# Performance work log

Measured on AMD Instinct MI355X. Metric: run time of the kernel, lower is better.

Reference implementation:

```python
import jax, jax.numpy as jnp
import numpy as np

DIM = 256
NUM_HEADS = 8
HEAD_DIM = DIM // NUM_HEADS
NUM_MAIN = 2
NUM_MOD = 4
SEQ_MAIN = 1536
SEQ_AUX = 768
BS = 2


def setup_inputs() -> dict:
    key = jax.random.key(0)
    ks = jax.random.split(key, 6)
    x0 = jax.random.normal(ks[0], (BS, SEQ_MAIN, DIM), jnp.float32)
    x1 = jax.random.normal(ks[1], (BS, SEQ_MAIN, DIM), jnp.float32)
    x2 = jax.random.normal(ks[2], (BS, SEQ_AUX, DIM), jnp.float32)
    x3 = jax.random.normal(ks[3], (BS, SEQ_AUX, DIM), jnp.float32)
    Wqkv = jax.random.normal(ks[4], (NUM_MOD, DIM, 3 * DIM), jnp.float32) * 0.02
    bqkv = jnp.zeros((NUM_MOD, 3 * DIM), jnp.float32)
    Wproj = jax.random.normal(ks[5], (NUM_MOD, DIM, DIM), jnp.float32) * 0.02
    bproj = jnp.zeros((NUM_MOD, DIM), jnp.float32)
    return {"x0": x0, "x1": x1, "x2": x2, "x3": x3,
            "Wqkv": Wqkv, "bqkv": bqkv, "Wproj": Wproj, "bproj": bproj}


def _split_qkv(qkv):
    bs, s, _ = qkv.shape
    qkv = qkv.reshape(bs, s, 3, NUM_HEADS, HEAD_DIM).transpose(2, 0, 3, 1, 4)
    return qkv[0], qkv[1], qkv[2]


def _sdpa(q, k, v):
    scale = 1.0 / jnp.sqrt(jnp.asarray(HEAD_DIM, q.dtype))
    scores = jnp.einsum('bhqd,bhkd->bhqk', q, k) * scale
    probs = jax.nn.softmax(scores, axis=-1)
    return jnp.einsum('bhqk,bhkd->bhqd', probs, v)


def _merge_heads(t):
    # [bs, heads, s, head_dim] -> [bs, s, dim]
    bs, h, s, d = t.shape
    return t.transpose(0, 2, 1, 3).reshape(bs, s, h * d)


def reference(x0, x1, x2, x3, Wqkv, bqkv, Wproj, bproj):
    xs = [x0, x1, x2, x3]
    seqlens = [x.shape[1] for x in xs]
    qs, ks, vs = [], [], []
    for i in range(NUM_MOD):
        q, k, v = _split_qkv(xs[i] @ Wqkv[i] + bqkv[i])
        qs.append(q); ks.append(k); vs.append(v)

    main_q = jnp.concatenate(qs[:NUM_MAIN], axis=2)
    main_k = jnp.concatenate(ks[:NUM_MAIN], axis=2)
    main_v = jnp.concatenate(vs[:NUM_MAIN], axis=2)
    main_x = _merge_heads(_sdpa(main_q, main_k, main_v))  # [bs, sum(main seqlens), dim]
    splits = np.cumsum(seqlens[:NUM_MAIN])[:-1]
    outs = list(jnp.split(main_x, splits, axis=1))

    # aux modalities attend over detached main KV + own KV
    mk = jax.lax.stop_gradient(main_k)
    mv = jax.lax.stop_gradient(main_v)
    for i in range(NUM_MAIN, NUM_MOD):
        k = jnp.concatenate([mk, ks[i]], axis=2)
        v = jnp.concatenate([mv, vs[i]], axis=2)
        outs.append(_merge_heads(_sdpa(qs[i], k, v)))

    outs = [outs[i] @ Wproj[i] + bproj[i] for i in range(NUM_MOD)]
    # concatenate per-modality outputs along the sequence dim for a single output
    return jnp.concatenate(outs, axis=1)
```

## Files before the change

### kernel.cpp

```cpp
#include <hip/hip_runtime.h>
#include <hip/hip_bf16.h>
#include <math.h>

#define BS 2
#define NHEADS 8
#define HD 32
#define DIM 256
#define W3 768
#define S_MAIN 1536
#define S_AUX 768
#define SM_TOT 3072
#define S_TOT 4608

typedef _Float16 f16x8 __attribute__((ext_vector_type(8)));
typedef _Float16 f16x4 __attribute__((ext_vector_type(4)));
typedef float    f32x4 __attribute__((ext_vector_type(4)));

#define QK_SCALE 0.25503491f

#define QM_H  0
#define KM_H  1572864
#define VMT_H 3145728
#define QA_H  4718592
#define KA_H  5505024
#define VAT_H 6291456
#define XH_H  7077888
#define AO0_F 3538944
#define AO1_F 5898240
#define L0_F  8257536
#define L1_F  8266752
#define WT1_H 16551936
#define WT2_H 17338368

#define GLOAD_LDS(SRC, DST)                                                    \
    __builtin_amdgcn_global_load_lds(                                          \
        (const __attribute__((address_space(1))) void*)(SRC),                  \
        (__attribute__((address_space(3))) void*)(DST), 16, 0, 0)

__global__ __launch_bounds__(256) void convert_kernel(
    const float* __restrict__ x0, const float* __restrict__ x1,
    const float* __restrict__ x2, const float* __restrict__ x3,
    const float* __restrict__ Wqkv, const float* __restrict__ Wproj,
    _Float16* __restrict__ wsh)
{
    const int bid = blockIdx.x;
    const int t   = threadIdx.x;

    if (bid < 1152) {
        const float* src;
        int off;
        if (bid < 384)      { src = x0; off = (bid      ) * 2048; }
        else if (bid < 768) { src = x1 - 786432 + 0;  off = bid * 2048; }
        else if (bid < 960) { src = x2; off = 1572864 + (bid - 768) * 2048; }
        else                { src = x3; off = 1966080 + (bid - 960) * 2048; }
        const int base = (bid < 384) ? bid * 2048
                       : (bid < 768) ? (bid - 384) * 2048
                       : (bid < 960) ? (bid - 768) * 2048
                       : (bid - 960) * 2048;
        const float* p = ((bid < 384) ? x0 : (bid < 768) ? x1
                         : (bid < 960) ? x2 : x3) + base + t * 8;
        _Float16* dst = wsh + XH_H + off + t * 8;
        const float4 u0 = *(const float4*)(p + 0);
        const float4 u1 = *(const float4*)(p + 4);
        f16x8 h;
        h[0] = (_Float16)u0.x; h[1] = (_Float16)u0.y;
        h[2] = (_Float16)u0.z; h[3] = (_Float16)u0.w;
        h[4] = (_Float16)u1.x; h[5] = (_Float16)u1.y;
        h[6] = (_Float16)u1.z; h[7] = (_Float16)u1.w;
        *(f16x8*)dst = h;
    } else if (bid < 1200) {
        const int i  = bid - 1152;
        const int m  = i / 12;
        const int cc = i % 12;
        const int col = cc * 64 + (t & 63);
        const int kq  = t >> 6;
        const float* Wm = Wqkv + m * (DIM * W3);
        _Float16*   Wt  = wsh + WT1_H + m * (W3 * DIM) + col * DIM;
        #pragma unroll 4
        for (int k = kq * 64; k < kq * 64 + 64; ++k)
            Wt[k] = (_Float16)Wm[k * W3 + col];
    } else {
        const int i  = bid - 1200;
        const int m  = i / 4;
        const int cc = i % 4;
        const int col = cc * 64 + (t & 63);
        const int kq  = t >> 6;
        const float* Wm = Wproj + m * (DIM * DIM);
        _Float16*   Wt  = wsh + WT2_H + m * (DIM * DIM) + col * DIM;
        #pragma unroll 4
        for (int k = kq * 64; k < kq * 64 + 64; ++k)
            Wt[k] = (_Float16)Wm[k * DIM + col];
    }
}

__global__ __launch_bounds__(256) void qkv_mfma_kernel(
    const _Float16* __restrict__ wsh_ro, const float* __restrict__ bqkv,
    _Float16* __restrict__ wsh)
{
    const int m  = blockIdx.z;
    const int rt = blockIdx.y;
    const int ct = blockIdx.x;
    const int s_m   = (m < 2) ? S_MAIN : S_AUX;
    const int nrows = BS * s_m;
    const int r0 = rt * 128;
    if (r0 >= nrows) return;

    const int xoff = (m == 0) ? 0 : (m == 1) ? 786432
                   : (m == 2) ? 1572864 : 1966080;
    const _Float16* xh = wsh_ro + XH_H + xoff;
    const _Float16* Wt = wsh_ro + WT1_H + m * (W3 * DIM);
    const float* bias  = bqkv + m * W3;

    __shared__ _Float16 As[128][40];
    __shared__ _Float16 Bs[64][40];

    const int t    = threadIdx.x;
    const int wid  = t >> 6;
    const int lane = t & 63;
    const int g    = lane >> 4;
    const int c    = lane & 15;
    const int c0   = ct * 64;

    const int arow = t >> 1;
    const int ak   = (t & 1) << 4;
    const int bcol = t & 63;
    const int bkg  = t >> 6;
    const int bsg  = bkg ^ ((bcol >> 3) & 3);

    f32x4 acc[2][4];
    #pragma unroll
    for (int i = 0; i < 2; ++i)
        #pragma unroll
        for (int j = 0; j < 4; ++j)
            acc[i][j] = (f32x4){0.f, 0.f, 0.f, 0.f};

    const _Float16* xp = xh + (r0 + arow) * DIM + ak;
    const _Float16* wp = Wt + (c0 + bcol) * DIM;

    for (int kk = 0; kk < DIM; kk += 32) {
        {
            const f16x8 h0 = *(const f16x8*)(xp + kk);
            const f16x8 h1 = *(const f16x8*)(xp + kk + 8);
            *(f16x8*)&As[arow][ak]     = h0;
            *(f16x8*)&As[arow][ak + 8] = h1;
        }
        {
            const f16x8 hb = *(const f16x8*)(wp + kk + bkg * 8);
            *(f16x8*)&Bs[bcol][bsg << 3] = hb;
        }
        __syncthreads();
        const f16x8 af0 = *(const f16x8*)&As[wid * 32 + c][g * 8];
        const f16x8 af1 = *(const f16x8*)&As[wid * 32 + 16 + c][g * 8];
        #pragma unroll
        for (int j = 0; j < 4; ++j) {
            const int bc = j * 16 + c;
            const int gg = g ^ ((bc >> 3) & 3);
            const f16x8 bf = *(const f16x8*)&Bs[bc][gg * 8];
            acc[0][j] = __builtin_amdgcn_mfma_f32_16x16x32_f16(af0, bf, acc[0][j], 0, 0, 0);
            acc[1][j] = __builtin_amdgcn_mfma_f32_16x16x32_f16(af1, bf, acc[1][j], 0, 0, 0);
        }
        __syncthreads();
    }

    #pragma unroll
    for (int i = 0; i < 2; ++i) {
        const int gr = r0 + wid * 32 + i * 16 + 4 * g;
        const int b  = (gr >= s_m) ? 1 : 0;
        const int s  = gr - (b ? s_m : 0);
        #pragma unroll
        for (int j = 0; j < 4; ++j) {
            const int col   = c0 + j * 16 + c;
            const int which = col >> 8;
            const int head  = (col >> 5) & 7;
            const int dd    = col & 31;
            const float bv  = bias[col];
            const f32x4 a   = acc[i][j];
            if (which < 2) {
                const float qs = (which == 0) ? QK_SCALE : 1.0f;
                _Float16* dst;
                int base;
                if (m < 2) {
                    dst  = wsh + (which == 0 ? QM_H : KM_H);
                    base = ((b * NHEADS + head) * SM_TOT + (s + m * S_MAIN)) * HD + dd;
                } else {
                    dst  = wsh + (which == 0 ? QA_H : KA_H);
                    base = ((((m - 2) * BS + b) * NHEADS + head) * S_AUX + s) * HD + dd;
                }
                dst[base + 0 * HD] = (_Float16)((a[0] + bv) * qs);
                dst[base + 1 * HD] = (_Float16)((a[1] + bv) * qs);
                dst[base + 2 * HD] = (_Float16)((a[2] + bv) * qs);
                dst[base + 3 * HD] = (_Float16)((a[3] + bv) * qs);
            } else {
                _Float16* dst;
                int base;
                if (m < 2) {
                    dst  = wsh + VMT_H;
                    base = ((b * NHEADS + head) * HD + dd) * SM_TOT + (s + m * S_MAIN);
                } else {
                    dst  = wsh + VAT_H;
                    base = ((((m - 2) * BS + b) * NHEADS + head) * HD + dd) * S_AUX + s;
                }
                f16x4 hv;
                hv[0] = (_Float16)(a[0] + bv);
                hv[1] = (_Float16)(a[1] + bv);
                hv[2] = (_Float16)(a[2] + bv);
                hv[3] = (_Float16)(a[3] + bv);
                *(f16x4*)(dst + base) = hv;
            }
        }
    }
}

__global__ __launch_bounds__(256) void attn_mfma_kernel(
    const _Float16* __restrict__ wsh, float* __restrict__ wsf)
{
    __shared__ _Float16 kbuf[2][64 * 32];
    __shared__ _Float16 vbuf[2][32 * 64];

    const int wid  = threadIdx.x >> 6;
    const int lane = threadIdx.x & 63;
    const int g    = lane >> 4;
    const int c    = lane & 15;

    const int bid = blockIdx.x;

    const _Float16 *qp, *kp0, *vt0, *kp1, *vt1;
    int n0, n1, vs1, orow0, ocol, half;

    if (bid < 384) {
        const int mbhg = bid / 12;
        const int mod  = mbhg >> 4;
        const int b    = (mbhg >> 3) & 1;
        const int h    = mbhg & 7;
        const int t    = bid % 12;
        const int qt   = t >> 1;
        half = t & 1;
        const int q0   = qt * 128 + wid * 32;
        const int mbh  = (mod * BS + b) * NHEADS + h;
        const int bh   = b * NHEADS + h;
        qp = wsh + QA_H + (mbh * S_AUX + q0) * HD;
        if (half == 0) {
            kp0 = wsh + KM_H  + bh * SM_TOT * HD;
            vt0 = wsh + VMT_H + bh * HD * SM_TOT;
            n0  = 1920;
            kp1 = nullptr; vt1 = nullptr; n1 = 0; vs1 = 0;
        } else {
            kp0 = wsh + KM_H  + (bh * SM_TOT + 1920) * HD;
            vt0 = wsh + VMT_H + bh * HD * SM_TOT + 1920;
            n0  = 1152;
            kp1 = wsh + KA_H  + mbh * S_AUX * HD;
            vt1 = wsh + VAT_H + mbh * HD * S_AUX;
            n1  = S_AUX; vs1 = S_AUX;
        }
        orow0 = b * S_TOT + SM_TOT + mod * S_AUX + q0;
        ocol  = h * HD;
    } else {
        const int idx = bid - 384;
        const int bh  = idx / 48;
        const int t   = idx % 48;
        const int qt  = t >> 1;
        half = t & 1;
        const int q0  = qt * 128 + wid * 32;
        const int b = bh >> 3, h = bh & 7;
        const int ks = half * 1536;
        qp  = wsh + QM_H  + (bh * SM_TOT + q0) * HD;
        kp0 = wsh + KM_H  + (bh * SM_TOT + ks) * HD;
        vt0 = wsh + VMT_H + bh * HD * SM_TOT + ks;
        n0  = 1536;
        kp1 = nullptr; vt1 = nullptr; n1 = 0; vs1 = 0;
        orow0 = b * S_TOT + q0;
        ocol  = h * HD;
    }

    const f16x8 qfA = *(const f16x8*)(qp + c * HD + g * 8);
    const f16x8 qfB = *(const f16x8*)(qp + (16 + c) * HD + g * 8);

    const int pc    = ((c >> 2) << 3) + (c & 3);
    const int kchr  = (g ^ (c >> 2)) << 3;
    const int koff0 = pc * HD + kchr;
    const int koff1 = (pc + 4) * HD + kchr;

    const int krow  = wid * 16 + (lane >> 2);
    const int kchg  = ((lane & 3) ^ ((krow >> 3) & 3)) << 3;

    const int srow = wid * 8 + (lane >> 3);
    const int jl   = lane & 7;
    const int vswz = (jl ^ (srow & 7)) << 3;
    const int vr0 = ((g     ^ (c & 7)) << 3);
    const int vr1 = (((g+4) ^ (c & 7)) << 3);

    f16x8 ones;
    #pragma unroll
    for (int i = 0; i < 8; ++i) ones[i] = (_Float16)1.0f;

    f32x4 otA0 = {0.f, 0.f, 0.f, 0.f}, otA1 = {0.f, 0.f, 0.f, 0.f};
    f32x4 otB0 = {0.f, 0.f, 0.f, 0.f}, otB1 = {0.f, 0.f, 0.f, 0.f};
    f32x4 ltA  = {0.f, 0.f, 0.f, 0.f}, ltB  = {0.f, 0.f, 0.f, 0.f};

    int cur = 0;

    #pragma unroll 1
    for (int seg = 0; seg < 2; ++seg) {
        const _Float16* kp_ = seg ? kp1 : kp0;
        const _Float16* vt_ = seg ? vt1 : vt0;
        const int n  = seg ? n1  : n0;
        const int vs = seg ? vs1 : SM_TOT;
        if (n == 0) break;

        #define STAGE(BI, K0)                                                  \
            {                                                                  \
                const _Float16* ks_ = kp_ + (K0 + krow) * HD + kchg;           \
                GLOAD_LDS(ks_, &kbuf[BI][wid * 512]);                          \
                const _Float16* vs_ = vt_ + (K0) + srow * vs + vswz;           \
                GLOAD_LDS(vs_, &vbuf[BI][wid * 512]);                          \
            }

        #define COMPUTE_TILE(BI)                                               \
            {                                                                  \
                const _Float16* kb_ = &kbuf[BI][0];                            \
                const _Float16* vb_ = &vbuf[BI][0];                            \
                const f16x8 kf0 = *(const f16x8*)(kb_ + koff0);                \
                const f16x8 kf1 = *(const f16x8*)(kb_ + koff1);                \
                const f16x8 kf2 = *(const f16x8*)(kb_ + 32 * HD + koff0);      \
                const f16x8 kf3 = *(const f16x8*)(kb_ + 32 * HD + koff1);      \
                const f16x8 va0 = *(const f16x8*)(vb_ + c * 64 + vr0);         \
                const f16x8 va1 = *(const f16x8*)(vb_ + (16 + c) * 64 + vr0);  \
                const f16x8 vb0 = *(const f16x8*)(vb_ + c * 64 + vr1);         \
                const f16x8 vb1 = *(const f16x8*)(vb_ + (16 + c) * 64 + vr1);  \
                f32x4 sA0 = __builtin_amdgcn_mfma_f32_16x16x32_f16(            \
                    kf0, qfA, (f32x4){0.f, 0.f, 0.f, 0.f}, 0, 0, 0);           \
                f32x4 sA1 = __builtin_amdgcn_mfma_f32_16x16x32_f16(            \
                    kf1, qfA, (f32x4){0.f, 0.f, 0.f, 0.f}, 0, 0, 0);           \
                f32x4 sA2 = __builtin_amdgcn_mfma_f32_16x16x32_f16(            \
                    kf2, qfA, (f32x4){0.f, 0.f, 0.f, 0.f}, 0, 0, 0);           \
                f32x4 sA3 = __builtin_amdgcn_mfma_f32_16x16x32_f16(            \
                    kf3, qfA, (f32x4){0.f, 0.f, 0.f, 0.f}, 0, 0, 0);           \
                f32x4 sB0 = __builtin_amdgcn_mfma_f32_16x16x32_f16(            \
                    kf0, qfB, (f32x4){0.f, 0.f, 0.f, 0.f}, 0, 0, 0);           \
                f32x4 sB1 = __builtin_amdgcn_mfma_f32_16x16x32_f16(            \
                    kf1, qfB, (f32x4){0.f, 0.f, 0.f, 0.f}, 0, 0, 0);           \
                f32x4 sB2 = __builtin_amdgcn_mfma_f32_16x16x32_f16(            \
                    kf2, qfB, (f32x4){0.f, 0.f, 0.f, 0.f}, 0, 0, 0);           \
                f32x4 sB3 = __builtin_amdgcn_mfma_f32_16x16x32_f16(            \
                    kf3, qfB, (f32x4){0.f, 0.f, 0.f, 0.f}, 0, 0, 0);           \
                float pA0[4], pA1[4], pA2[4], pA3[4];                          \
                float pB0[4], pB1[4], pB2[4], pB3[4];                          \
                _Pragma("unroll")                                              \
                for (int r = 0; r < 4; ++r) {                                  \
                    pA0[r] = __builtin_amdgcn_exp2f(sA0[r]);                   \
                    pA1[r] = __builtin_amdgcn_exp2f(sA1[r]);                   \
                    pA2[r] = __builtin_amdgcn_exp2f(sA2[r]);                   \
                    pA3[r] = __builtin_amdgcn_exp2f(sA3[r]);                   \
                    pB0[r] = __builtin_amdgcn_exp2f(sB0[r]);                   \
                    pB1[r] = __builtin_amdgcn_exp2f(sB1[r]);                   \
                    pB2[r] = __builtin_amdgcn_exp2f(sB2[r]);                   \
                    pB3[r] = __builtin_amdgcn_exp2f(sB3[r]);                   \
                }                                                              \
                f16x8 pbA0, pbA1, pbB0, pbB1;                                  \
                _Pragma("unroll")                                              \
                for (int r = 0; r < 4; ++r) {                                  \
                    pbA0[r]     = (_Float16)pA0[r];                            \
                    pbA0[r + 4] = (_Float16)pA1[r];                            \
                    pbA1[r]     = (_Float16)pA2[r];                            \
                    pbA1[r + 4] = (_Float16)pA3[r];                            \
                    pbB0[r]     = (_Float16)pB0[r];                            \
                    pbB0[r + 4] = (_Float16)pB1[r];                            \
                    pbB1[r]     = (_Float16)pB2[r];                            \
                    pbB1[r + 4] = (_Float16)pB3[r];                            \
                }                                                              \
                ltA = __builtin_amdgcn_mfma_f32_16x16x32_f16(ones, pbA0, ltA, 0, 0, 0); \
                ltA = __builtin_amdgcn_mfma_f32_16x16x32_f16(ones, pbA1, ltA, 0, 0, 0); \
                ltB = __builtin_amdgcn_mfma_f32_16x16x32_f16(ones, pbB0, ltB, 0, 0, 0); \
                ltB = __builtin_amdgcn_mfma_f32_16x16x32_f16(ones, pbB1, ltB, 0, 0, 0); \
                otA0 = __builtin_amdgcn_mfma_f32_16x16x32_f16(va0, pbA0, otA0, 0, 0, 0); \
                otA1 = __builtin_amdgcn_mfma_f32_16x16x32_f16(va1, pbA0, otA1, 0, 0, 0); \
                otB0 = __builtin_amdgcn_mfma_f32_16x16x32_f16(va0, pbB0, otB0, 0, 0, 0); \
                otB1 = __builtin_amdgcn_mfma_f32_16x16x32_f16(va1, pbB0, otB1, 0, 0, 0); \
                otA0 = __builtin_amdgcn_mfma_f32_16x16x32_f16(vb0, pbA1, otA0, 0, 0, 0); \
                otA1 = __builtin_amdgcn_mfma_f32_16x16x32_f16(vb1, pbA1, otA1, 0, 0, 0); \
                otB0 = __builtin_amdgcn_mfma_f32_16x16x32_f16(vb0, pbB1, otB0, 0, 0, 0); \
                otB1 = __builtin_amdgcn_mfma_f32_16x16x32_f16(vb1, pbB1, otB1, 0, 0, 0); \
            }

        STAGE(cur, 0);
        __syncthreads();

        #pragma unroll 1
        for (int k0 = 0; k0 < n; k0 += 64) {
            if (k0 + 64 < n)
                STAGE(cur ^ 1, k0 + 64);
            COMPUTE_TILE(cur);
            __syncthreads();
            cur ^= 1;
        }

        #undef STAGE
        #undef COMPUTE_TILE
    }

    float* aoBase = wsf + (half ? AO1_F : AO0_F);
    float* lBase  = wsf + (half ? L1_F  : L0_F);

    float* aoA = aoBase + (orow0 + c) * DIM + ocol;
    float* aoB = aoBase + (orow0 + 16 + c) * DIM + ocol;
    float4 w0, w1, w2, w3;
    w0.x = otA0[0]; w0.y = otA0[1]; w0.z = otA0[2]; w0.w = otA0[3];
    w1.x = otA1[0]; w1.y = otA1[1]; w1.z = otA1[2]; w1.w = otA1[3];
    w2.x = otB0[0]; w2.y = otB0[1]; w2.z = otB0[2]; w2.w = otB0[3];
    w3.x = otB1[0]; w3.y = otB1[1]; w3.z = otB1[2]; w3.w = otB1[3];
    *(float4*)(aoA + 4 * g)      = w0;
    *(float4*)(aoA + 16 + 4 * g) = w1;
    *(float4*)(aoB + 4 * g)      = w2;
    *(float4*)(aoB + 16 + 4 * g) = w3;

    if (g == 0) {
        lBase[orow0 + c]      = ltA[0];
        lBase[orow0 + 16 + c] = ltB[0];
    }
}

__global__ __launch_bounds__(256) void proj_mfma_kernel(
    const float* __restrict__ wsf, const _Float16* __restrict__ wsh_ro,
    const float* __restrict__ bproj, float* __restrict__ out)
{
    const int ct = blockIdx.x;
    const int rt = blockIdx.y;
    const int r0 = rt * 128, c0 = ct * 64;
    const int seq = r0 % S_TOT;
    const int mod = (seq < S_MAIN) ? 0 : (seq < SM_TOT) ? 1
                  : (seq < SM_TOT + S_AUX) ? 2 : 3;
    const _Float16* Wt = wsh_ro + WT2_H + mod * (DIM * DIM);
    const float* bias  = bproj + mod * DIM;
    const float* A0    = wsf + AO0_F;
    const float* A1    = wsf + AO1_F;
    const float* L0p   = wsf + L0_F;
    const float* L1p   = wsf + L1_F;

    __shared__ _Float16 As[128][40];
    __shared__ _Float16 Bs[64][40];
    __shared__ float Linv[128];

    const int t    = threadIdx.x;
    const int wid  = t >> 6;
    const int lane = t & 63;
    const int g    = lane >> 4;
    const int c    = lane & 15;

    if (t < 128) Linv[t] = 1.0f / (L0p[r0 + t] + L1p[r0 + t]);
    __syncthreads();

    const int arow = t >> 1;
    const int ak   = (t & 1) << 4;
    const int bcol = t & 63;
    const int bkg  = t >> 6;
    const int bsg  = bkg ^ ((bcol >> 3) & 3);
    const float linv_r = Linv[arow];

    f32x4 acc[2][4];
    #pragma unroll
    for (int i = 0; i < 2; ++i)
        #pragma unroll
        for (int j = 0; j < 4; ++j)
            acc[i][j] = (f32x4){0.f, 0.f, 0.f, 0.f};

    const float* pa0 = A0 + (r0 + arow) * DIM + ak;
    const float* pa1 = A1 + (r0 + arow) * DIM + ak;
    const _Float16* wp = Wt + (c0 + bcol) * DIM;

    for (int kk = 0; kk < DIM; kk += 32) {
        {
            const float4 u0 = *(const float4*)(pa0 + kk + 0);
            const float4 u1 = *(const float4*)(pa0 + kk + 4);
            const float4 u2 = *(const float4*)(pa0 + kk + 8);
            const float4 u3 = *(const float4*)(pa0 + kk + 12);
            const float4 v0 = *(const float4*)(pa1 + kk + 0);
            const float4 v1 = *(const float4*)(pa1 + kk + 4);
            const float4 v2 = *(const float4*)(pa1 + kk + 8);
            const float4 v3 = *(const float4*)(pa1 + kk + 12);
            f16x8 h0, h1;
            h0[0] = (_Float16)((u0.x + v0.x) * linv_r);
            h0[1] = (_Float16)((u0.y + v0.y) * linv_r);
            h0[2] = (_Float16)((u0.z + v0.z) * linv_r);
            h0[3] = (_Float16)((u0.w + v0.w) * linv_r);
            h0[4] = (_Float16)((u1.x + v1.x) * linv_r);
            h0[5] = (_Float16)((u1.y + v1.y) * linv_r);
            h0[6] = (_Float16)((u1.z + v1.z) * linv_r);
            h0[7] = (_Float16)((u1.w + v1.w) * linv_r);
            h1[0] = (_Float16)((u2.x + v2.x) * linv_r);
            h1[1] = (_Float16)((u2.y + v2.y) * linv_r);
            h1[2] = (_Float16)((u2.z + v2.z) * linv_r);
            h1[3] = (_Float16)((u2.w + v2.w) * linv_r);
            h1[4] = (_Float16)((u3.x + v3.x) * linv_r);
            h1[5] = (_Float16)((u3.y + v3.y) * linv_r);
            h1[6] = (_Float16)((u3.z + v3.z) * linv_r);
            h1[7] = (_Float16)((u3.w + v3.w) * linv_r);
            *(f16x8*)&As[arow][ak]     = h0;
            *(f16x8*)&As[arow][ak + 8] = h1;
        }
        {
            const f16x8 hb = *(const f16x8*)(wp + kk + bkg * 8);
            *(f16x8*)&Bs[bcol][bsg << 3] = hb;
        }
        __syncthreads();
        const f16x8 af0 = *(const f16x8*)&As[wid * 32 + c][g * 8];
        const f16x8 af1 = *(const f16x8*)&As[wid * 32 + 16 + c][g * 8];
        #pragma unroll
        for (int j = 0; j < 4; ++j) {
            const int bc = j * 16 + c;
            const int gg = g ^ ((bc >> 3) & 3);
            const f16x8 bf = *(const f16x8*)&Bs[bc][gg * 8];
            acc[0][j] = __builtin_amdgcn_mfma_f32_16x16x32_f16(af0, bf, acc[0][j], 0, 0, 0);
            acc[1][j] = __builtin_amdgcn_mfma_f32_16x16x32_f16(af1, bf, acc[1][j], 0, 0, 0);
        }
        __syncthreads();
    }

    #pragma unroll
    for (int i = 0; i < 2; ++i) {
        const int gr = r0 + wid * 32 + i * 16 + 4 * g;
        #pragma unroll
        for (int j = 0; j < 4; ++j) {
            const int col  = c0 + j * 16 + c;
            const float bv = bias[col];
            const f32x4 a  = acc[i][j];
            out[(gr + 0) * DIM + col] = a[0] + bv;
            out[(gr + 1) * DIM + col] = a[1] + bv;
            out[(gr + 2) * DIM + col] = a[2] + bv;
            out[(gr + 3) * DIM + col] = a[3] + bv;
        }
    }
}

extern "C" void kernel_launch(void* const* d_in, const int* in_sizes, int n_in,
                              void* d_out, int out_size, void* d_ws, size_t ws_size,
                              hipStream_t stream)
{
    const float* x0    = (const float*)d_in[0];
    const float* x1    = (const float*)d_in[1];
    const float* x2    = (const float*)d_in[2];
    const float* x3    = (const float*)d_in[3];
    const float* Wqkv  = (const float*)d_in[4];
    const float* bqkv  = (const float*)d_in[5];
    const float* Wproj = (const float*)d_in[6];
    const float* bproj = (const float*)d_in[7];
    _Float16* wsh = (_Float16*)d_ws;
    float*    wsf = (float*)d_ws;
    float*    out = (float*)d_out;

    convert_kernel<<<dim3(1216), 256, 0, stream>>>(
        x0, x1, x2, x3, Wqkv, Wproj, wsh);

    qkv_mfma_kernel<<<dim3(12, 24, 4), 256, 0, stream>>>(wsh, bqkv, wsh);

    attn_mfma_kernel<<<dim3(1152), 256, 0, stream>>>(wsh, wsf);

    proj_mfma_kernel<<<dim3(4, 72), 256, 0, stream>>>(wsf, wsh, bproj, out);
}
```

Measured before the change: 101.7 us.

## Tile weight transpose through LDS and double KV tile per attention barrier

The weight conversion now transposes 64x64 tiles through shared memory, so both the global reads and the fp16 writes are coalesced. The old version wrote one element per thread with a column stride, and this change uses more blocks to do it. The attention loop now stages and computes two 64-key tiles per iteration, which halves the number of __syncthreads barriers and doubles the shared-memory K/V buffers. Key segment lengths must be multiples of 128, which holds for 3072 and 768.

```diff
diff --git a/kernel.cpp b/kernel.cpp
--- a/kernel.cpp
+++ b/kernel.cpp
@@ -43,23 +43,20 @@
     const float* __restrict__ Wqkv, const float* __restrict__ Wproj,
     _Float16* __restrict__ wsh)
 {
+    __shared__ _Float16 tl[64][65];
     const int bid = blockIdx.x;
     const int t   = threadIdx.x;
 
     if (bid < 1152) {
-        const float* src;
-        int off;
-        if (bid < 384)      { src = x0; off = (bid      ) * 2048; }
-        else if (bid < 768) { src = x1 - 786432 + 0;  off = bid * 2048; }
-        else if (bid < 960) { src = x2; off = 1572864 + (bid - 768) * 2048; }
-        else                { src = x3; off = 1966080 + (bid - 960) * 2048; }
         const int base = (bid < 384) ? bid * 2048
                        : (bid < 768) ? (bid - 384) * 2048
                        : (bid < 960) ? (bid - 768) * 2048
                        : (bid - 960) * 2048;
+        const int off  = (bid < 768) ? bid * 2048
+                       : (bid < 960) ? 1572864 + (bid - 768) * 2048
+                       : 1966080 + (bid - 960) * 2048;
         const float* p = ((bid < 384) ? x0 : (bid < 768) ? x1
                          : (bid < 960) ? x2 : x3) + base + t * 8;
-        _Float16* dst = wsh + XH_H + off + t * 8;
         const float4 u0 = *(const float4*)(p + 0);
         const float4 u1 = *(const float4*)(p + 4);
         f16x8 h;
@@ -67,29 +64,44 @@
         h[2] = (_Float16)u0.z; h[3] = (_Float16)u0.w;
         h[4] = (_Float16)u1.x; h[5] = (_Float16)u1.y;
         h[6] = (_Float16)u1.z; h[7] = (_Float16)u1.w;
-        *(f16x8*)dst = h;
-    } else if (bid < 1200) {
-        const int i  = bid - 1152;
-        const int m  = i / 12;
-        const int cc = i % 12;
-        const int col = cc * 64 + (t & 63);
-        const int kq  = t >> 6;
-        const float* Wm = Wqkv + m * (DIM * W3);
-        _Float16*   Wt  = wsh + WT1_H + m * (W3 * DIM) + col * DIM;
-        #pragma unroll 4
-        for (int k = kq * 64; k < kq * 64 + 64; ++k)
-            Wt[k] = (_Float16)Wm[k * W3 + col];
+        *(f16x8*)(wsh + XH_H + off + t * 8) = h;
     } else {
-        const int i  = bid - 1200;
-        const int m  = i / 4;
-        const int cc = i % 4;
-        const int col = cc * 64 + (t & 63);
-        const int kq  = t >> 6;
-        const float* Wm = Wproj + m * (DIM * DIM);
-        _Float16*   Wt  = wsh + WT2_H + m * (DIM * DIM) + col * DIM;
-        #pragma unroll 4
-        for (int k = kq * 64; k < kq * 64 + 64; ++k)
-            Wt[k] = (_Float16)Wm[k * DIM + col];
+        const float* Wsrc;
+        _Float16*    Wdst;
+        int ldw, kt, ct;
+        if (bid < 1344) {
+            const int i = bid - 1152;
+            const int m = i / 48;
+            const int r = i % 48;
+            kt = r / 12; ct = r % 12;
+            Wsrc = Wqkv + m * (DIM * W3);
+            Wdst = wsh + WT1_H + m * (W3 * DIM);
+            ldw  = W3;
+        } else {
+            const int i = bid - 1344;
+            const int m = i / 16;
+            const int r = i % 16;
+            kt = r / 4; ct = r % 4;
+            Wsrc = Wproj + m * (DIM * DIM);
+            Wdst = wsh + WT2_H + m * (DIM * DIM);
+            ldw  = DIM;
+        }
+        #pragma unroll
+        for (int rr = 0; rr < 16; ++rr) {
+            const int row = rr * 4 + (t >> 6);
+            tl[row][t & 63] =
+                (_Float16)Wsrc[(kt * 64 + row) * ldw + ct * 64 + (t & 63)];
+        }
+        __syncthreads();
+        #pragma unroll
+        for (int rr = 0; rr < 2; ++rr) {
+            const int col = rr * 32 + (t >> 3);
+            const int kc  = (t & 7) * 8;
+            f16x8 v;
+            #pragma unroll
+            for (int i2 = 0; i2 < 8; ++i2) v[i2] = tl[kc + i2][col];
+            *(f16x8*)(Wdst + (ct * 64 + col) * DIM + kt * 64 + kc) = v;
+        }
     }
 }
 
@@ -214,8 +226,8 @@
 __global__ __launch_bounds__(256) void attn_mfma_kernel(
     const _Float16* __restrict__ wsh, float* __restrict__ wsf)
 {
-    __shared__ _Float16 kbuf[2][64 * 32];
-    __shared__ _Float16 vbuf[2][32 * 64];
+    __shared__ _Float16 kbuf[2][2][64 * 32];
+    __shared__ _Float16 vbuf[2][2][32 * 64];
 
     const int wid  = threadIdx.x >> 6;
     const int lane = threadIdx.x & 63;
@@ -307,18 +319,18 @@
         const int vs = seg ? vs1 : SM_TOT;
         if (n == 0) break;
 
-        #define STAGE(BI, K0)                                                  \
+        #define STAGE(BI, S, K0)                                               \
             {                                                                  \
                 const _Float16* ks_ = kp_ + (K0 + krow) * HD + kchg;           \
-                GLOAD_LDS(ks_, &kbuf[BI][wid * 512]);                          \
+                GLOAD_LDS(ks_, &kbuf[BI][S][wid * 512]);                       \
                 const _Float16* vs_ = vt_ + (K0) + srow * vs + vswz;           \
-                GLOAD_LDS(vs_, &vbuf[BI][wid * 512]);                          \
+                GLOAD_LDS(vs_, &vbuf[BI][S][wid * 512]);                       \
             }
 
-        #define COMPUTE_TILE(BI)                                               \
+        #define COMPUTE_TILE(BI, S)                                            \
             {                                                                  \
-                const _Float16* kb_ = &kbuf[BI][0];                            \
-                const _Float16* vb_ = &vbuf[BI][0];                            \
+                const _Float16* kb_ = &kbuf[BI][S][0];                         \
+                const _Float16* vb_ = &vbuf[BI][S][0];                         \
                 const f16x8 kf0 = *(const f16x8*)(kb_ + koff0);                \
                 const f16x8 kf1 = *(const f16x8*)(kb_ + koff1);                \
                 const f16x8 kf2 = *(const f16x8*)(kb_ + 32 * HD + koff0);      \
@@ -382,14 +394,18 @@
                 otB1 = __builtin_amdgcn_mfma_f32_16x16x32_f16(vb1, pbB1, otB1, 0, 0, 0); \
             }
 
-        STAGE(cur, 0);
+        STAGE(cur, 0, 0);
+        STAGE(cur, 1, 64);
         __syncthreads();
 
         #pragma unroll 1
-        for (int k0 = 0; k0 < n; k0 += 64) {
-            if (k0 + 64 < n)
-                STAGE(cur ^ 1, k0 + 64);
-            COMPUTE_TILE(cur);
+        for (int k0 = 0; k0 < n; k0 += 128) {
+            if (k0 + 128 < n) {
+                STAGE(cur ^ 1, 0, k0 + 128);
+                STAGE(cur ^ 1, 1, k0 + 192);
+            }
+            COMPUTE_TILE(cur, 0);
+            COMPUTE_TILE(cur, 1);
             __syncthreads();
             cur ^= 1;
         }
@@ -547,7 +563,7 @@
     float*    wsf = (float*)d_ws;
     float*    out = (float*)d_out;
 
-    convert_kernel<<<dim3(1216), 256, 0, stream>>>(
+    convert_kernel<<<dim3(1408), 256, 0, stream>>>(
         x0, x1, x2, x3, Wqkv, Wproj, wsh);
 
     qkv_mfma_kernel<<<dim3(12, 24, 4), 256, 0, stream>>>(wsh, bqkv, wsh);
```

Result: faster. 94.92 us (-6.7%).
